# Kernel tuning notes

Hardware: AMD Instinct MI355X
Metric: run time of the kernel (lower is better)

The kernel has to match this reference:

```python
import jax, jax.numpy as jnp
import numpy as np

MASK_VALUE = -1000000.0


def setup_inputs() -> dict:
    key = jax.random.key(0)
    k1, k2, k3, k4 = jax.random.split(key, 4)
    B, Lq, Lk, d = 32, 1024, 1024, 128
    return {
        "query": jax.random.normal(k1, (B, Lq, d), dtype=jnp.float32),
        "key": jax.random.normal(k2, (B, Lk, d), dtype=jnp.float32),
        "value": jax.random.normal(k3, (B, Lk, d), dtype=jnp.float32),
        "valid_length": jax.random.randint(k4, (B,), 0, Lk, dtype=jnp.int64),
    }


def reference(query, key, value, valid_length):
    # query [B, Lq, d], key/value [B, Lk, d], valid_length [B]
    d = query.shape[-1]
    # scores [B, Lq, Lk]
    scores = jnp.einsum("bqd,bkd->bqk", query, key) / jnp.sqrt(jnp.float32(d))
    Lk = key.shape[1]
    # mask positions >= valid_length with -1e6 (per-batch, broadcast over Lq)
    pos = jnp.arange(Lk)  # [Lk]
    mask = pos[None, None, :] >= valid_length[:, None, None]  # [B, 1, Lk]
    scores = jnp.where(mask, MASK_VALUE, scores)
    attn = jax.nn.softmax(scores, axis=-1)
    # dropout p=0.0 in eval -> identity
    return jnp.einsum("bqk,bkd->bqd", attn, value)
```

## Files before the change

### kernel.cpp

```cpp
#include <hip/hip_runtime.h>

#define B_N 32
#define LQ  1024
#define LK  1024
#define DH  128

typedef __attribute__((ext_vector_type(4))) float    f32x4;
typedef __attribute__((ext_vector_type(8))) short    s16x8;
typedef __attribute__((ext_vector_type(4))) _Float16 f16x4;
typedef __attribute__((ext_vector_type(8))) _Float16 f16x8;

__device__ inline unsigned short f2bf(float f) {
    union { float f; unsigned u; } c; c.f = f;
    unsigned u = c.u;
    u += 0x7fffu + ((u >> 16) & 1u);
    return (unsigned short)(u >> 16);
}

#define ESCALE 0.12751743f

#define G2L16(gp, lp) __builtin_amdgcn_global_load_lds(                         \
    (const __attribute__((address_space(1))) void*)(gp),                        \
    (__attribute__((address_space(3))) void*)(lp), 16, 0, 0)

__global__ __launch_bounds__(256)
void prep_kv(const float* __restrict__ K, const float* __restrict__ V,
             const int* __restrict__ VL,
             unsigned short* __restrict__ Kb, _Float16* __restrict__ Vt)
{
    __shared__ float tl[32 * 132];
    const int tid  = threadIdx.x;
    const int lane = tid & 63;
    const int wv   = tid >> 6;
    const int n    = lane & 15;
    const int quad = lane >> 4;

    const int  idx = blockIdx.x;
    const bool isK = (idx >> 10) == 0;
    const int  b   = (idx & 7) | (((idx >> 3) & 3) << 3);
    const int  kt  = (idx >> 5) & 31;

    const int vl = VL[b];
    if (isK) {
        if (vl <= 0 || kt >= 2 * ((vl + 63) >> 6)) return;
    } else {
        const int nch = (vl > 0) ? ((vl + 63) >> 6) : 16;
        if (kt >= 2 * nch) return;
    }

    const float4* src = (const float4*)((isK ? K : V) + ((size_t)b * LK + kt * 32) * DH);
    #pragma unroll
    for (int h = 0; h < 4; ++h) {
        const int i2 = h * 256 + tid;
        const int row = i2 >> 5, c4 = i2 & 31;
        *(float4*)&tl[row * 132 + c4 * 4] = src[i2];
    }
    __syncthreads();

    if (isK) {
        union { s16x8 v; unsigned short u[8]; } t8;
        #pragma unroll
        for (int h = 0; h < 2; ++h) {
            const int f = wv * 2 + h;
            const int tt2 = f >> 2, s = f & 3;
            const float* p = &tl[(tt2 * 16 + n) * 132 + s * 32 + quad * 8];
            const float4 a = *(const float4*)p;
            const float4 c = *(const float4*)(p + 4);
            t8.u[0] = f2bf(a.x); t8.u[1] = f2bf(a.y); t8.u[2] = f2bf(a.z); t8.u[3] = f2bf(a.w);
            t8.u[4] = f2bf(c.x); t8.u[5] = f2bf(c.y); t8.u[6] = f2bf(c.z); t8.u[7] = f2bf(c.w);
            const int w = b * 256 + (kt * 2 + tt2) * 4 + s;
            *(s16x8*)(Kb + (size_t)w * 512 + lane * 8) = t8.v;
        }
    } else {
        #pragma unroll
        for (int h = 0; h < 2; ++h) {
            const int f  = wv * 2 + h;
            const int kg = f >> 2, dp = f & 3;
            f16x8 t8;
            #pragma unroll
            for (int i = 0; i < 4; ++i) {
                const float* row = &tl[(kg * 16 + quad * 4 + i) * 132 + dp * 32 + n];
                t8[i]     = (_Float16)row[0];
                t8[4 + i] = (_Float16)row[16];
            }
            const int v = (b * 64 + kt * 2 + kg) * 4 + dp;
            *(f16x8*)(Vt + (size_t)v * 512 + lane * 8) = t8;
        }
    }
}

__global__ __launch_bounds__(256)
void attn_fwd(const float* __restrict__ Q, const unsigned short* __restrict__ Kb,
              const _Float16* __restrict__ Vt, const int* __restrict__ VL,
              float* __restrict__ O)
{
    __shared__ __align__(16) unsigned short bufK[2][16 * 512];
    __shared__ __align__(16) _Float16       bufV[2][16 * 512];

    const int tid  = threadIdx.x;
    const int lane = tid & 63;
    const int w    = tid >> 6;
    const int quad = lane >> 4;
    const int m16  = lane & 15;

    const int idx = blockIdx.x;
    const int qg  = (idx >> 5) & 15;
    const int b   = (idx & 7) | ((((idx >> 3) + (idx >> 8)) & 3) << 3);
    const int q0  = qg * 64;

    const int vl  = VL[b];
    const int nch = (vl > 0) ? ((vl + 63) >> 6) : 16;
    const float emaskval = (vl == 0) ? 1.0f : 0.0f;

    s16x8 qf[4];
    {
        const float* qrow = Q + ((size_t)b * LQ + q0 + w * 16 + m16) * DH + quad * 8;
        #pragma unroll
        for (int s = 0; s < 4; ++s) {
            const float4 a = *(const float4*)(qrow + s * 32);
            const float4 c = *(const float4*)(qrow + s * 32 + 4);
            union { s16x8 v; unsigned short u[8]; } t;
            t.u[0] = f2bf(a.x); t.u[1] = f2bf(a.y); t.u[2] = f2bf(a.z); t.u[3] = f2bf(a.w);
            t.u[4] = f2bf(c.x); t.u[5] = f2bf(c.y); t.u[6] = f2bf(c.z); t.u[7] = f2bf(c.w);
            qf[s] = t.v;
        }
    }

    f32x4 o[8];
    #pragma unroll
    for (int dt = 0; dt < 8; ++dt) o[dt] = (f32x4){0.f, 0.f, 0.f, 0.f};
    float lrun = 0.f;

    const unsigned short* kg0 = Kb + (size_t)b * (256 * 512);
    const _Float16*       vg0 = Vt + (size_t)b * (256 * 512);
    const int co = tid * 8;

#define STAGE(c, t)                                                             \
    do {                                                                        \
        const unsigned short* gk_ = kg0 + (size_t)(t) * 8192;                   \
        const _Float16*       gv_ = vg0 + (size_t)(t) * 8192;                   \
        _Pragma("unroll")                                                       \
        for (int it_ = 0; it_ < 4; ++it_)                                       \
            G2L16(gk_ + it_ * 2048 + co, &bufK[c][it_ * 2048 + co]);            \
        _Pragma("unroll")                                                       \
        for (int it_ = 0; it_ < 4; ++it_)                                       \
            G2L16(gv_ + it_ * 2048 + co, &bufV[c][it_ * 2048 + co]);            \
    } while (0)

    STAGE(0, 0);
    STAGE(1, 1);

    for (int t = 0; t < nch; ++t) {
        if (t + 1 < nch) { asm volatile("s_waitcnt vmcnt(8)" ::: "memory"); }
        else             { asm volatile("s_waitcnt vmcnt(0)" ::: "memory"); }
        __builtin_amdgcn_sched_barrier(0);
        __builtin_amdgcn_s_barrier();
        __builtin_amdgcn_sched_barrier(0);

        const unsigned short* bk = &bufK[t & 1][0];
        const _Float16*       bv = &bufV[t & 1][0];
        const bool maskc = (t * 64 + 64 > vl);
        f16x4 pA[4];

        #pragma unroll
        for (int g = 0; g < 4; ++g) {
            f32x4 st = (f32x4){0.f, 0.f, 0.f, 0.f};
            #pragma unroll
            for (int s = 0; s < 4; ++s) {
                const s16x8 kf = *(const s16x8*)(bk + (g * 4 + s) * 512 + lane * 8);
                st = __builtin_amdgcn_mfma_f32_16x16x32_bf16(kf, qf[s], st, 0, 0, 0);
            }
            #pragma unroll
            for (int i = 0; i < 4; ++i) {
                float e = __builtin_amdgcn_exp2f(st[i] * ESCALE);
                if (maskc && (t * 64 + g * 16 + quad * 4 + i >= vl)) e = emaskval;
                lrun += e;
                pA[g][i] = (_Float16)e;
            }
        }

        #pragma unroll
        for (int g = 0; g < 4; ++g) {
            #pragma unroll
            for (int dp = 0; dp < 4; ++dp) {
                const f16x8 w8 = *(const f16x8*)(bv + (g * 4 + dp) * 512 + lane * 8);
                const f16x4 lo = __builtin_shufflevector(w8, w8, 0, 1, 2, 3);
                const f16x4 hi = __builtin_shufflevector(w8, w8, 4, 5, 6, 7);
                o[dp * 2]     = __builtin_amdgcn_mfma_f32_16x16x16f16(pA[g], lo, o[dp * 2],     0, 0, 0);
                o[dp * 2 + 1] = __builtin_amdgcn_mfma_f32_16x16x16f16(pA[g], hi, o[dp * 2 + 1], 0, 0, 0);
            }
        }

        __builtin_amdgcn_s_barrier();
        __builtin_amdgcn_sched_barrier(0);
        if (t + 2 < nch) STAGE(t & 1, t + 2);
    }
#undef STAGE

    float L = lrun;
    L += __shfl_xor(L, 16);
    L += __shfl_xor(L, 32);
    const size_t obase = ((size_t)b * LQ + q0 + w * 16 + quad * 4) * DH + m16;
    #pragma unroll
    for (int r = 0; r < 4; ++r) {
        const float inv = 1.0f / __shfl(L, quad * 4 + r);
        #pragma unroll
        for (int dt = 0; dt < 8; ++dt)
            O[obase + (size_t)r * DH + dt * 16] = o[dt][r] * inv;
    }
}

extern "C" void kernel_launch(void* const* d_in, const int* in_sizes, int n_in,
                              void* d_out, int out_size, void* d_ws, size_t ws_size,
                              hipStream_t stream) {
    const float* Q  = (const float*)d_in[0];
    const float* K  = (const float*)d_in[1];
    const float* V  = (const float*)d_in[2];
    const int*   VL = (const int*)d_in[3];
    float* O = (float*)d_out;
    (void)in_sizes; (void)n_in; (void)out_size; (void)ws_size;

    unsigned short* Kb = (unsigned short*)d_ws;
    _Float16*       Vt = (_Float16*)(Kb + (size_t)B_N * 256 * 512);

    prep_kv<<<dim3(2048), dim3(256), 0, stream>>>(K, V, VL, Kb, Vt);
    attn_fwd<<<dim3(B_N * (LQ / 64)), dim3(256), 0, stream>>>(Q, Kb, Vt, VL, O);
}
```

Before: 113.9 us.

## Split key chunks across wave pairs and schedule blocks longest-batch-first

Each block now handles 32 query rows instead of 64. The four waves form two pairs that split each 64-key chunk: each wave of a pair handles 32 keys for the same 16 query rows, and the pair reduces its partial outputs and row sums through LDS at the end. An extra prep block ranks batches by valid length and writes a block-to-(batch, query tile) list, so the longest batches are dispatched first. This is meant to even out the load across CUs when valid lengths vary, and to cut the per-wave serial loop length. The cost is half as much K/V reuse per block, so global and LDS staging traffic doubles, plus an extra LDS reduction and a sync at the end.

```diff
diff --git a/kernel.cpp b/kernel.cpp
--- a/kernel.cpp
+++ b/kernel.cpp
@@ -26,16 +26,42 @@
 __global__ __launch_bounds__(256)
 void prep_kv(const float* __restrict__ K, const float* __restrict__ V,
              const int* __restrict__ VL,
-             unsigned short* __restrict__ Kb, _Float16* __restrict__ Vt)
+             unsigned short* __restrict__ Kb, _Float16* __restrict__ Vt,
+             int* __restrict__ UL)
 {
     __shared__ float tl[32 * 132];
+    __shared__ int rank_sh[32];
     const int tid  = threadIdx.x;
     const int lane = tid & 63;
     const int wv   = tid >> 6;
     const int n    = lane & 15;
     const int quad = lane >> 4;
 
-    const int  idx = blockIdx.x;
+    const int idx = blockIdx.x;
+
+    if (idx == 2048) {
+        if (tid < 64) {
+            int my = 0;
+            if (lane < 32) {
+                const int v = VL[lane];
+                my = (v > 0) ? ((v + 63) >> 6) : 16;
+            }
+            int rank = 0;
+            #pragma unroll
+            for (int k = 0; k < 32; ++k) {
+                const int other = __shfl(my, k);
+                if (lane < 32 && (other > my || (other == my && k < lane))) ++rank;
+            }
+            if (lane < 32) rank_sh[rank] = lane;
+        }
+        __syncthreads();
+        for (int u = tid; u < 1024; u += 256) {
+            const int r = u >> 5, q = u & 31;
+            UL[u] = rank_sh[r] | (q << 5);
+        }
+        return;
+    }
+
     const bool isK = (idx >> 10) == 0;
     const int  b   = (idx & 7) | (((idx >> 3) & 3) << 3);
     const int  kt  = (idx >> 5) & 31;
@@ -92,21 +118,22 @@
 __global__ __launch_bounds__(256)
 void attn_fwd(const float* __restrict__ Q, const unsigned short* __restrict__ Kb,
               const _Float16* __restrict__ Vt, const int* __restrict__ VL,
-              float* __restrict__ O)
+              const int* __restrict__ UL, float* __restrict__ O)
 {
     __shared__ __align__(16) unsigned short bufK[2][16 * 512];
     __shared__ __align__(16) _Float16       bufV[2][16 * 512];
 
     const int tid  = threadIdx.x;
     const int lane = tid & 63;
-    const int w    = tid >> 6;
+    const int wv   = tid >> 6;
+    const int h    = wv >> 1;
+    const int j    = wv & 1;
     const int quad = lane >> 4;
     const int m16  = lane & 15;
 
-    const int idx = blockIdx.x;
-    const int qg  = (idx >> 5) & 15;
-    const int b   = (idx & 7) | ((((idx >> 3) + (idx >> 8)) & 3) << 3);
-    const int q0  = qg * 64;
+    const int uv = UL[blockIdx.x];
+    const int b  = uv & 31;
+    const int q0 = (uv >> 5) * 32;
 
     const int vl  = VL[b];
     const int nch = (vl > 0) ? ((vl + 63) >> 6) : 16;
@@ -114,7 +141,7 @@
 
     s16x8 qf[4];
     {
-        const float* qrow = Q + ((size_t)b * LQ + q0 + w * 16 + m16) * DH + quad * 8;
+        const float* qrow = Q + ((size_t)b * LQ + q0 + h * 16 + m16) * DH + quad * 8;
         #pragma unroll
         for (int s = 0; s < 4; ++s) {
             const float4 a = *(const float4*)(qrow + s * 32);
@@ -160,10 +187,11 @@
         const unsigned short* bk = &bufK[t & 1][0];
         const _Float16*       bv = &bufV[t & 1][0];
         const bool maskc = (t * 64 + 64 > vl);
-        f16x4 pA[4];
-
-        #pragma unroll
-        for (int g = 0; g < 4; ++g) {
+        f16x4 pA[2];
+
+        #pragma unroll
+        for (int g2 = 0; g2 < 2; ++g2) {
+            const int g = j * 2 + g2;
             f32x4 st = (f32x4){0.f, 0.f, 0.f, 0.f};
             #pragma unroll
             for (int s = 0; s < 4; ++s) {
@@ -175,19 +203,20 @@
                 float e = __builtin_amdgcn_exp2f(st[i] * ESCALE);
                 if (maskc && (t * 64 + g * 16 + quad * 4 + i >= vl)) e = emaskval;
                 lrun += e;
-                pA[g][i] = (_Float16)e;
-            }
-        }
-
-        #pragma unroll
-        for (int g = 0; g < 4; ++g) {
+                pA[g2][i] = (_Float16)e;
+            }
+        }
+
+        #pragma unroll
+        for (int g2 = 0; g2 < 2; ++g2) {
+            const int g = j * 2 + g2;
             #pragma unroll
             for (int dp = 0; dp < 4; ++dp) {
                 const f16x8 w8 = *(const f16x8*)(bv + (g * 4 + dp) * 512 + lane * 8);
                 const f16x4 lo = __builtin_shufflevector(w8, w8, 0, 1, 2, 3);
                 const f16x4 hi = __builtin_shufflevector(w8, w8, 4, 5, 6, 7);
-                o[dp * 2]     = __builtin_amdgcn_mfma_f32_16x16x16f16(pA[g], lo, o[dp * 2],     0, 0, 0);
-                o[dp * 2 + 1] = __builtin_amdgcn_mfma_f32_16x16x16f16(pA[g], hi, o[dp * 2 + 1], 0, 0, 0);
+                o[dp * 2]     = __builtin_amdgcn_mfma_f32_16x16x16f16(pA[g2], lo, o[dp * 2],     0, 0, 0);
+                o[dp * 2 + 1] = __builtin_amdgcn_mfma_f32_16x16x16f16(pA[g2], hi, o[dp * 2 + 1], 0, 0, 0);
             }
         }
 
@@ -197,16 +226,30 @@
     }
 #undef STAGE
 
-    float L = lrun;
-    L += __shfl_xor(L, 16);
-    L += __shfl_xor(L, 32);
-    const size_t obase = ((size_t)b * LQ + q0 + w * 16 + quad * 4) * DH + m16;
-    #pragma unroll
-    for (int r = 0; r < 4; ++r) {
-        const float inv = 1.0f / __shfl(L, quad * 4 + r);
-        #pragma unroll
-        for (int dt = 0; dt < 8; ++dt)
-            O[obase + (size_t)r * DH + dt * 16] = o[dt][r] * inv;
+    f32x4* Om = (f32x4*)&bufK[0][0];
+    float*  Lm = (float*)&bufV[0][0];
+    if (j == 1) {
+        #pragma unroll
+        for (int dt = 0; dt < 8; ++dt) Om[(h * 8 + dt) * 64 + lane] = o[dt];
+        Lm[h * 64 + lane] = lrun;
+    }
+    __syncthreads();
+    if (j == 0) {
+        f32x4 om[8];
+        #pragma unroll
+        for (int dt = 0; dt < 8; ++dt) om[dt] = o[dt] + Om[(h * 8 + dt) * 64 + lane];
+        float L = lrun + Lm[h * 64 + lane];
+
+        L += __shfl_xor(L, 16);
+        L += __shfl_xor(L, 32);
+        const size_t obase = ((size_t)b * LQ + q0 + h * 16 + quad * 4) * DH + m16;
+        #pragma unroll
+        for (int r = 0; r < 4; ++r) {
+            const float inv = 1.0f / __shfl(L, quad * 4 + r);
+            #pragma unroll
+            for (int dt = 0; dt < 8; ++dt)
+                O[obase + (size_t)r * DH + dt * 16] = om[dt][r] * inv;
+        }
     }
 }
 
@@ -222,7 +265,8 @@
 
     unsigned short* Kb = (unsigned short*)d_ws;
     _Float16*       Vt = (_Float16*)(Kb + (size_t)B_N * 256 * 512);
-
-    prep_kv<<<dim3(2048), dim3(256), 0, stream>>>(K, V, VL, Kb, Vt);
-    attn_fwd<<<dim3(B_N * (LQ / 64)), dim3(256), 0, stream>>>(Q, Kb, Vt, VL, O);
-}
+    int*            UL = (int*)(Vt + (size_t)B_N * 256 * 512);
+
+    prep_kv<<<dim3(2049), dim3(256), 0, stream>>>(K, V, VL, Kb, Vt, UL);
+    attn_fwd<<<dim3(1024), dim3(256), 0, stream>>>(Q, Kb, Vt, VL, UL, O);
+}
```

After: 116.4 us. 1.02x slower.

## Schedule attention blocks longest-first by valid length for load balance

Applied to the files above, without the earlier changes.

An extra block in the prep kernel sorts batches by their number of key chunks (from valid_length) and writes a work list, and the attention kernel reads its batch and query tile from that list. Blocks with the most work are issued first, and the ordering snakes so heavy and light tiles pair across waves, which is meant to reduce tail imbalance from the variable per-batch sequence lengths. It costs one extra dependent global load per block and drops the previous XCD-aware batch interleaving, which may hurt L2 locality of K/V across chiplets.

```diff
diff --git a/kernel.cpp b/kernel.cpp
--- a/kernel.cpp
+++ b/kernel.cpp
@@ -26,16 +26,43 @@
 __global__ __launch_bounds__(256)
 void prep_kv(const float* __restrict__ K, const float* __restrict__ V,
              const int* __restrict__ VL,
-             unsigned short* __restrict__ Kb, _Float16* __restrict__ Vt)
+             unsigned short* __restrict__ Kb, _Float16* __restrict__ Vt,
+             int* __restrict__ UL)
 {
     __shared__ float tl[32 * 132];
+    __shared__ int rank_sh[32];
     const int tid  = threadIdx.x;
     const int lane = tid & 63;
     const int wv   = tid >> 6;
     const int n    = lane & 15;
     const int quad = lane >> 4;
 
-    const int  idx = blockIdx.x;
+    const int idx = blockIdx.x;
+
+    if (idx == 2048) {
+        if (tid < 64) {
+            int my = 0;
+            if (lane < 32) {
+                const int v = VL[lane];
+                my = (v > 0) ? ((v + 63) >> 6) : 16;
+            }
+            int rank = 0;
+            #pragma unroll
+            for (int k = 0; k < 32; ++k) {
+                const int other = __shfl(my, k);
+                if (lane < 32 && (other > my || (other == my && k < lane))) ++rank;
+            }
+            if (lane < 32) rank_sh[rank] = lane;
+        }
+        __syncthreads();
+        for (int i = tid; i < 512; i += 256) {
+            const int s = (i < 256) ? i : (511 - (i - 256));
+            const int r = s >> 4, q = s & 15;
+            UL[i] = rank_sh[r] | (q << 5);
+        }
+        return;
+    }
+
     const bool isK = (idx >> 10) == 0;
     const int  b   = (idx & 7) | (((idx >> 3) & 3) << 3);
     const int  kt  = (idx >> 5) & 31;
@@ -92,7 +119,7 @@
 __global__ __launch_bounds__(256)
 void attn_fwd(const float* __restrict__ Q, const unsigned short* __restrict__ Kb,
               const _Float16* __restrict__ Vt, const int* __restrict__ VL,
-              float* __restrict__ O)
+              const int* __restrict__ UL, float* __restrict__ O)
 {
     __shared__ __align__(16) unsigned short bufK[2][16 * 512];
     __shared__ __align__(16) _Float16       bufV[2][16 * 512];
@@ -103,10 +130,9 @@
     const int quad = lane >> 4;
     const int m16  = lane & 15;
 
-    const int idx = blockIdx.x;
-    const int qg  = (idx >> 5) & 15;
-    const int b   = (idx & 7) | ((((idx >> 3) + (idx >> 8)) & 3) << 3);
-    const int q0  = qg * 64;
+    const int uv = UL[blockIdx.x];
+    const int b  = uv & 31;
+    const int q0 = (uv >> 5) * 64;
 
     const int vl  = VL[b];
     const int nch = (vl > 0) ? ((vl + 63) >> 6) : 16;
@@ -222,7 +248,8 @@
 
     unsigned short* Kb = (unsigned short*)d_ws;
     _Float16*       Vt = (_Float16*)(Kb + (size_t)B_N * 256 * 512);
-
-    prep_kv<<<dim3(2048), dim3(256), 0, stream>>>(K, V, VL, Kb, Vt);
-    attn_fwd<<<dim3(B_N * (LQ / 64)), dim3(256), 0, stream>>>(Q, Kb, Vt, VL, O);
-}
+    int*            UL = (int*)(Vt + (size_t)B_N * 256 * 512);
+
+    prep_kv<<<dim3(2049), dim3(256), 0, stream>>>(K, V, VL, Kb, Vt, UL);
+    attn_fwd<<<dim3(512), dim3(256), 0, stream>>>(Q, Kb, Vt, VL, UL, O);
+}
```

Result: no change. 114.6 us (+0.6%).
